# Optimization experiments

Hardware: AMD Instinct MI355X
Metric: run time of the kernel (lower is better)

Reference implementation:

```python
import jax, jax.numpy as jnp
import numpy as np

EPS = 0.1        # entropic regularization
MAX_ITER = 50    # fixed iteration count (torch early-stops on host; we run all iters)
P = 1            # cost exponent
N_POINTS = 4096
D_FEAT = 2


def _cost_matrix(x, y):
    # x: [N, D], y: [M, D] -> C: [N, M], sum_d |x_i - y_j|^p
    return jnp.sum(jnp.abs(x[:, None, :] - y[None, :, :]) ** P, axis=-1)


def setup_inputs() -> dict:
    key = jax.random.key(0)
    k1, k2 = jax.random.split(key)
    x = jax.random.normal(k1, (N_POINTS, D_FEAT), dtype=jnp.float32)
    y = jax.random.normal(k2, (N_POINTS, D_FEAT), dtype=jnp.float32)
    return {"x": x, "y": y}


def reference(x, y):
    n, m = x.shape[0], y.shape[0]
    C = _cost_matrix(x, y)  # [N, M]
    log_mu = jnp.log(jnp.full((n,), 1.0 / n, dtype=x.dtype) + 1e-8)
    log_nu = jnp.log(jnp.full((m,), 1.0 / m, dtype=y.dtype) + 1e-8)

    def M(u, v):
        # modified cost: (-C + u_i + v_j) / eps
        return (-C + u[:, None] + v[None, :]) / EPS

    def step(carry, _):
        u, v = carry
        u = EPS * (log_mu - jax.scipy.special.logsumexp(M(u, v), axis=-1)) + u
        v = EPS * (log_nu - jax.scipy.special.logsumexp(M(u, v), axis=-2)) + v
        return (u, v), None

    u0 = jnp.zeros((n,), dtype=x.dtype)
    v0 = jnp.zeros((m,), dtype=y.dtype)
    (u, v), _ = jax.lax.scan(step, (u0, v0), None, length=MAX_ITER)

    pi = jnp.exp(M(u, v))                 # transport plan [N, M]
    cost = jnp.sum(pi * C)                # scalar (reduction='none', 2D input)
    return cost ** (1.0 / P), pi, C
```

## Files before the change

### kernel.cpp

```cpp
#include <hip/hip_runtime.h>


#define NPTS    4096
#define EPS_F   0.1f
#define S_L2E   14.426950408889634f
#define INV_SL  0.0693147180559945f
#define A_LOGMU (-0.8317725207f)
#define N_ITER  50
#define NBLK    256
#define TPB     1024
#define WPB     (TPB / 64)
#define RPW     2
#define HALFC   2048
#define NJT     (HALFC / 256)
#define NLEAF   16
#define BSTRIDE 64
#define BAR_INTS ((NLEAF + 2) * BSTRIDE)

typedef float f4u __attribute__((ext_vector_type(4), aligned(4)));

__device__ __forceinline__ float fexp2(float x) {
#if __has_builtin(__builtin_amdgcn_exp2f)
  return __builtin_amdgcn_exp2f(x);
#else
  float r;
  asm("v_exp_f32 %0, %1" : "=v"(r) : "v"(x));
  return r;
#endif
}

__device__ __forceinline__ float coh_load(const float* p) {
  return __hip_atomic_load(p, __ATOMIC_RELAXED, __HIP_MEMORY_SCOPE_AGENT);
}
__device__ __forceinline__ void coh_store(float* p, float x) {
  __hip_atomic_store(p, x, __ATOMIC_RELAXED, __HIP_MEMORY_SCOPE_AGENT);
}

__device__ __forceinline__ float wave_sum64(float x) {
#pragma unroll
  for (int off = 32; off > 0; off >>= 1) x += __shfl_xor(x, off, 64);
  return x;
}

__device__ __forceinline__ void grid_barrier(int* bar, int k) {
  __syncthreads();
  if (threadIdx.x == 0) {
    int* leaf = bar + (blockIdx.x & (NLEAF - 1)) * BSTRIDE;
    const int old = __hip_atomic_fetch_add(leaf, 1, __ATOMIC_RELAXED,
                                           __HIP_MEMORY_SCOPE_AGENT);
    if (old == NLEAF * k - 1) {
      int* root = bar + NLEAF * BSTRIDE;
      const int ro = __hip_atomic_fetch_add(root, 1, __ATOMIC_RELAXED,
                                            __HIP_MEMORY_SCOPE_AGENT);
      if (ro == NLEAF * k - 1)
        __hip_atomic_store(bar + (NLEAF + 1) * BSTRIDE, k, __ATOMIC_RELAXED,
                           __HIP_MEMORY_SCOPE_AGENT);
    }
    while (__hip_atomic_load(bar + (NLEAF + 1) * BSTRIDE, __ATOMIC_RELAXED,
                             __HIP_MEMORY_SCOPE_AGENT) < k)
      __builtin_amdgcn_s_sleep(2);
  }
  __syncthreads();
}

__device__ __forceinline__ void stage(const float* __restrict__ win,
                                      const float* __restrict__ colp,
                                      float* __restrict__ sW,
                                      float* __restrict__ sC0,
                                      float* __restrict__ sC1, int tid) {
  const int c = tid * 4;
  const float w0 = coh_load(win + c + 0), w1 = coh_load(win + c + 1);
  const float w2 = coh_load(win + c + 2), w3 = coh_load(win + c + 3);
  const float4 a = ((const float4*)colp)[(c >> 1) + 0];
  const float4 b = ((const float4*)colp)[(c >> 1) + 1];
  float4 W, C0, C1;
  W.x = w0 * S_L2E;  W.y = w1 * S_L2E;  W.z = w2 * S_L2E;  W.w = w3 * S_L2E;
  C0.x = a.x * S_L2E; C0.y = a.z * S_L2E; C0.z = b.x * S_L2E; C0.w = b.z * S_L2E;
  C1.x = a.y * S_L2E; C1.y = a.w * S_L2E; C1.z = b.y * S_L2E; C1.w = b.w * S_L2E;
  *(float4*)(sW + c)  = W;
  *(float4*)(sC0 + c) = C0;
  *(float4*)(sC1 + c) = C1;
  __syncthreads();
}

__device__ __forceinline__ void phase(const float* __restrict__ rx,
                                      const float* __restrict__ ry,
                                      const float* __restrict__ sW,
                                      const float* __restrict__ sC0,
                                      const float* __restrict__ sC1,
                                      float (*sPart)[RPW],
                                      float* __restrict__ wout,
                                      int row0blk, int wv, int lane, int tid) {
  const int base = (wv & 1) * HALFC + lane * 4;
  float acc0 = 0.f, acc1 = 0.f;
#pragma unroll
  for (int jt = 0; jt < NJT; ++jt) {
    const int j = base + jt * 256;
    const float4 W  = *(const float4*)(sW + j);
    const float4 C0 = *(const float4*)(sC0 + j);
    const float4 C1 = *(const float4*)(sC1 + j);
    {
      const float a0 = (W.x - fabsf(rx[0] - C0.x)) - fabsf(ry[0] - C1.x);
      const float a1 = (W.y - fabsf(rx[0] - C0.y)) - fabsf(ry[0] - C1.y);
      const float a2 = (W.z - fabsf(rx[0] - C0.z)) - fabsf(ry[0] - C1.z);
      const float a3 = (W.w - fabsf(rx[0] - C0.w)) - fabsf(ry[0] - C1.w);
      acc0 += (fexp2(a0) + fexp2(a1)) + (fexp2(a2) + fexp2(a3));
    }
    {
      const float a0 = (W.x - fabsf(rx[1] - C0.x)) - fabsf(ry[1] - C1.x);
      const float a1 = (W.y - fabsf(rx[1] - C0.y)) - fabsf(ry[1] - C1.y);
      const float a2 = (W.z - fabsf(rx[1] - C0.z)) - fabsf(ry[1] - C1.z);
      const float a3 = (W.w - fabsf(rx[1] - C0.w)) - fabsf(ry[1] - C1.w);
      acc1 += (fexp2(a0) + fexp2(a1)) + (fexp2(a2) + fexp2(a3));
    }
  }
  const float S0 = wave_sum64(acc0);
  const float S1 = wave_sum64(acc1);
  if (lane == 0) { sPart[wv][0] = S0; sPart[wv][1] = S1; }
  __syncthreads();
  if (tid < 16) {
    const int p = tid >> 1, r = tid & 1;
    const float S = sPart[2 * p][r] + sPart[2 * p + 1][r];
    coh_store(wout + row0blk + p * RPW + r, A_LOGMU - EPS_F * __logf(S));
  }
}

__global__ void __launch_bounds__(TPB, 4)
sinkhorn_main(const float* __restrict__ x, const float* __restrict__ y,
              float* __restrict__ u, float* __restrict__ v,
              float* __restrict__ out, int* __restrict__ bar) {
  __shared__ float sW[NPTS], sC0[NPTS], sC1[NPTS];
  __shared__ float sPart[WPB][RPW];
  __shared__ float sCost[WPB];

  const int tid  = threadIdx.x;
  const int wv   = tid >> 6;
  const int lane = tid & 63;
  const int row0blk = blockIdx.x * (WPB / 2) * RPW;
  const int row0 = row0blk + (wv >> 1) * RPW;

  float rxu[RPW], ryu[RPW], rxv[RPW], ryv[RPW];
#pragma unroll
  for (int r = 0; r < RPW; ++r) {
    const float2 xr = ((const float2*)x)[row0 + r];
    const float2 yr = ((const float2*)y)[row0 + r];
    rxu[r] = xr.x * S_L2E;  ryu[r] = xr.y * S_L2E;
    rxv[r] = yr.x * S_L2E;  ryv[r] = yr.y * S_L2E;
  }

  int k = 0;
  for (int it = 0; it < N_ITER; ++it) {
    stage(v, y, sW, sC0, sC1, tid);
    phase(rxu, ryu, sW, sC0, sC1, sPart, u, row0blk, wv, lane, tid);
    grid_barrier(bar, ++k);
    stage(u, x, sW, sC0, sC1, tid);
    phase(rxv, ryv, sW, sC0, sC1, sPart, v, row0blk, wv, lane, tid);
    grid_barrier(bar, ++k);
  }
  stage(v, y, sW, sC0, sC1, tid);

  float* __restrict__ pi = out + 1;
  float* __restrict__ cm = out + 1 + (size_t)NPTS * NPTS;
  float uu[RPW];
#pragma unroll
  for (int r = 0; r < RPW; ++r) uu[r] = coh_load(u + row0 + r) * S_L2E;

  const int base = (wv & 1) * HALFC + lane * 4;
  float costacc = 0.f;
#pragma unroll 2
  for (int jt = 0; jt < NJT; ++jt) {
    const int j = base + jt * 256;
    const float4 W  = *(const float4*)(sW + j);
    const float4 C0 = *(const float4*)(sC0 + j);
    const float4 C1 = *(const float4*)(sC1 + j);
#pragma unroll
    for (int r = 0; r < RPW; ++r) {
      const float s0 = fabsf(rxu[r] - C0.x) + fabsf(ryu[r] - C1.x);
      const float s1 = fabsf(rxu[r] - C0.y) + fabsf(ryu[r] - C1.y);
      const float s2 = fabsf(rxu[r] - C0.z) + fabsf(ryu[r] - C1.z);
      const float s3 = fabsf(rxu[r] - C0.w) + fabsf(ryu[r] - C1.w);
      const float p0 = fexp2((uu[r] + W.x) - s0);
      const float p1 = fexp2((uu[r] + W.y) - s1);
      const float p2 = fexp2((uu[r] + W.z) - s2);
      const float p3 = fexp2((uu[r] + W.w) - s3);
      costacc = fmaf(p0, s0, costacc);
      costacc = fmaf(p1, s1, costacc);
      costacc = fmaf(p2, s2, costacc);
      costacc = fmaf(p3, s3, costacc);
      const size_t off = (size_t)(row0 + r) * NPTS + j;
      f4u pv; pv.x = p0; pv.y = p1; pv.z = p2; pv.w = p3;
      f4u cv; cv.x = s0 * INV_SL; cv.y = s1 * INV_SL;
      cv.z = s2 * INV_SL; cv.w = s3 * INV_SL;
      *(f4u*)(pi + off) = pv;
      *(f4u*)(cm + off) = cv;
    }
  }
  const float cw = wave_sum64(costacc);
  if (lane == 0) sCost[wv] = cw;
  __syncthreads();
  if (tid == 0) {
    float c = 0.f;
#pragma unroll
    for (int w = 0; w < WPB; ++w) c += sCost[w];
    atomicAdd(out, c * INV_SL);
  }
}

__global__ void sinkhorn_init(float* __restrict__ v, int* __restrict__ bar,
                              float* __restrict__ out) {
  const int i = blockIdx.x * blockDim.x + threadIdx.x;
  if (i < NPTS) coh_store(v + i, 0.f);
  if (i < BAR_INTS)
    __hip_atomic_store(bar + i, 0, __ATOMIC_RELAXED, __HIP_MEMORY_SCOPE_AGENT);
  if (i == 0) out[0] = 0.f;
}

extern "C" void kernel_launch(void* const* d_in, const int* in_sizes, int n_in,
                              void* d_out, int out_size, void* d_ws, size_t ws_size,
                              hipStream_t stream) {
  const float* x = (const float*)d_in[0];
  const float* y = (const float*)d_in[1];
  float* u = (float*)d_ws;
  float* v = u + NPTS;
  int* bar = (int*)(v + NPTS);
  float* out = (float*)d_out;

  sinkhorn_init<<<dim3(16), dim3(256), 0, stream>>>(v, bar, out);

  void* args[6];
  args[0] = (void*)&x;
  args[1] = (void*)&y;
  args[2] = (void*)&u;
  args[3] = (void*)&v;
  args[4] = (void*)&out;
  args[5] = (void*)&bar;
  hipLaunchCooperativeKernel((void*)sinkhorn_main, dim3(NBLK), dim3(TPB),
                             args, 0, stream);
}
```

Measured before the change: 750.8 us.

## Cache row-phase cost tile in registers and stage coordinates once

Each thread computes its cost values for the u-update once and keeps them in 64 registers, so the u-phase no longer recomputes the absolute differences every iteration. The x and y coordinates are staged into separate shared-memory arrays once before the loop, and each iteration stages only the dual vector. The grid barrier now spreads the release flag across per-leaf replicas so waiting blocks poll different addresses, and it sleeps for a shorter interval. The cost is higher register pressure at 1024 threads per block and more shared memory, which could reduce occupancy or cause spills.

After: 700.7 us. -6.7%, faster.

```diff
diff --git a/kernel.cpp b/kernel.cpp
--- a/kernel.cpp
+++ b/kernel.cpp
@@ -15,7 +15,7 @@
 #define NJT     (HALFC / 256)
 #define NLEAF   16
 #define BSTRIDE 64
-#define BAR_INTS ((NLEAF + 2) * BSTRIDE)
+#define BAR_INTS ((NLEAF + 1 + NLEAF) * BSTRIDE)
 
 typedef float f4u __attribute__((ext_vector_type(4), aligned(4)));
 
@@ -52,46 +52,81 @@
       int* root = bar + NLEAF * BSTRIDE;
       const int ro = __hip_atomic_fetch_add(root, 1, __ATOMIC_RELAXED,
                                             __HIP_MEMORY_SCOPE_AGENT);
-      if (ro == NLEAF * k - 1)
-        __hip_atomic_store(bar + (NLEAF + 1) * BSTRIDE, k, __ATOMIC_RELAXED,
-                           __HIP_MEMORY_SCOPE_AGENT);
-    }
-    while (__hip_atomic_load(bar + (NLEAF + 1) * BSTRIDE, __ATOMIC_RELAXED,
+      if (ro == NLEAF * k - 1) {
+#pragma unroll
+        for (int rr = 0; rr < NLEAF; ++rr)
+          __hip_atomic_store(bar + (NLEAF + 1 + rr) * BSTRIDE, k,
+                             __ATOMIC_RELAXED, __HIP_MEMORY_SCOPE_AGENT);
+      }
+    }
+    int* rep = bar + (NLEAF + 1 + (blockIdx.x & (NLEAF - 1))) * BSTRIDE;
+    while (__hip_atomic_load(rep, __ATOMIC_RELAXED,
                              __HIP_MEMORY_SCOPE_AGENT) < k)
-      __builtin_amdgcn_s_sleep(2);
-  }
-  __syncthreads();
-}
-
-__device__ __forceinline__ void stage(const float* __restrict__ win,
-                                      const float* __restrict__ colp,
-                                      float* __restrict__ sW,
-                                      float* __restrict__ sC0,
-                                      float* __restrict__ sC1, int tid) {
+      __builtin_amdgcn_s_sleep(1);
+  }
+  __syncthreads();
+}
+
+__device__ __forceinline__ void stageW(const float* __restrict__ win,
+                                       float* __restrict__ sW, int tid) {
   const int c = tid * 4;
   const float w0 = coh_load(win + c + 0), w1 = coh_load(win + c + 1);
   const float w2 = coh_load(win + c + 2), w3 = coh_load(win + c + 3);
+  float4 W;
+  W.x = w0 * S_L2E;  W.y = w1 * S_L2E;  W.z = w2 * S_L2E;  W.w = w3 * S_L2E;
+  *(float4*)(sW + c) = W;
+  __syncthreads();
+}
+
+__device__ __forceinline__ void stageCoords(const float* __restrict__ colp,
+                                            float* __restrict__ sC0,
+                                            float* __restrict__ sC1, int tid) {
+  const int c = tid * 4;
   const float4 a = ((const float4*)colp)[(c >> 1) + 0];
   const float4 b = ((const float4*)colp)[(c >> 1) + 1];
-  float4 W, C0, C1;
-  W.x = w0 * S_L2E;  W.y = w1 * S_L2E;  W.z = w2 * S_L2E;  W.w = w3 * S_L2E;
+  float4 C0, C1;
   C0.x = a.x * S_L2E; C0.y = a.z * S_L2E; C0.z = b.x * S_L2E; C0.w = b.z * S_L2E;
   C1.x = a.y * S_L2E; C1.y = a.w * S_L2E; C1.z = b.y * S_L2E; C1.w = b.w * S_L2E;
-  *(float4*)(sW + c)  = W;
   *(float4*)(sC0 + c) = C0;
   *(float4*)(sC1 + c) = C1;
-  __syncthreads();
-}
-
-__device__ __forceinline__ void phase(const float* __restrict__ rx,
-                                      const float* __restrict__ ry,
-                                      const float* __restrict__ sW,
-                                      const float* __restrict__ sC0,
-                                      const float* __restrict__ sC1,
-                                      float (*sPart)[RPW],
-                                      float* __restrict__ wout,
-                                      int row0blk, int wv, int lane, int tid) {
-  const int base = (wv & 1) * HALFC + lane * 4;
+}
+
+__device__ __forceinline__ void phaseU(const float* __restrict__ sW,
+                                       const float (&Dreg)[NJT][RPW][4],
+                                       float (*sPart)[RPW],
+                                       float* __restrict__ wout,
+                                       int row0blk, int wv, int lane, int tid,
+                                       int base) {
+  float acc0 = 0.f, acc1 = 0.f;
+#pragma unroll
+  for (int jt = 0; jt < NJT; ++jt) {
+    const int j = base + jt * 256;
+    const float4 W = *(const float4*)(sW + j);
+    acc0 += (fexp2(W.x - Dreg[jt][0][0]) + fexp2(W.y - Dreg[jt][0][1])) +
+            (fexp2(W.z - Dreg[jt][0][2]) + fexp2(W.w - Dreg[jt][0][3]));
+    acc1 += (fexp2(W.x - Dreg[jt][1][0]) + fexp2(W.y - Dreg[jt][1][1])) +
+            (fexp2(W.z - Dreg[jt][1][2]) + fexp2(W.w - Dreg[jt][1][3]));
+  }
+  const float S0 = wave_sum64(acc0);
+  const float S1 = wave_sum64(acc1);
+  if (lane == 0) { sPart[wv][0] = S0; sPart[wv][1] = S1; }
+  __syncthreads();
+  if (tid < 16) {
+    const int p = tid >> 1, r = tid & 1;
+    const float S = sPart[2 * p][r] + sPart[2 * p + 1][r];
+    coh_store(wout + row0blk + p * RPW + r, A_LOGMU - EPS_F * __logf(S));
+  }
+}
+
+__device__ __forceinline__ void phaseV(const float* __restrict__ rx,
+                                       const float* __restrict__ ry,
+                                       const float* __restrict__ sW,
+                                       const float* __restrict__ sC0,
+                                       const float* __restrict__ sC1,
+                                       float (*sPart)[RPW],
+                                       float* __restrict__ wout,
+                                       int row0blk, int wv, int lane, int tid,
+                                       int base) {
   float acc0 = 0.f, acc1 = 0.f;
 #pragma unroll
   for (int jt = 0; jt < NJT; ++jt) {
@@ -129,7 +164,9 @@
 sinkhorn_main(const float* __restrict__ x, const float* __restrict__ y,
               float* __restrict__ u, float* __restrict__ v,
               float* __restrict__ out, int* __restrict__ bar) {
-  __shared__ float sW[NPTS], sC0[NPTS], sC1[NPTS];
+  __shared__ float sW[NPTS];
+  __shared__ float sC0y[NPTS], sC1y[NPTS];
+  __shared__ float sC0x[NPTS], sC1x[NPTS];
   __shared__ float sPart[WPB][RPW];
   __shared__ float sCost[WPB];
 
@@ -138,6 +175,7 @@
   const int lane = tid & 63;
   const int row0blk = blockIdx.x * (WPB / 2) * RPW;
   const int row0 = row0blk + (wv >> 1) * RPW;
+  const int base = (wv & 1) * HALFC + lane * 4;
 
   float rxu[RPW], ryu[RPW], rxv[RPW], ryv[RPW];
 #pragma unroll
@@ -148,16 +186,35 @@
     rxv[r] = yr.x * S_L2E;  ryv[r] = yr.y * S_L2E;
   }
 
+  stageCoords(y, sC0y, sC1y, tid);
+  stageCoords(x, sC0x, sC1x, tid);
+  __syncthreads();
+
+  float Dreg[NJT][RPW][4];
+#pragma unroll
+  for (int jt = 0; jt < NJT; ++jt) {
+    const int j = base + jt * 256;
+    const float4 C0 = *(const float4*)(sC0y + j);
+    const float4 C1 = *(const float4*)(sC1y + j);
+#pragma unroll
+    for (int r = 0; r < RPW; ++r) {
+      Dreg[jt][r][0] = fabsf(rxu[r] - C0.x) + fabsf(ryu[r] - C1.x);
+      Dreg[jt][r][1] = fabsf(rxu[r] - C0.y) + fabsf(ryu[r] - C1.y);
+      Dreg[jt][r][2] = fabsf(rxu[r] - C0.z) + fabsf(ryu[r] - C1.z);
+      Dreg[jt][r][3] = fabsf(rxu[r] - C0.w) + fabsf(ryu[r] - C1.w);
+    }
+  }
+
   int k = 0;
   for (int it = 0; it < N_ITER; ++it) {
-    stage(v, y, sW, sC0, sC1, tid);
-    phase(rxu, ryu, sW, sC0, sC1, sPart, u, row0blk, wv, lane, tid);
+    stageW(v, sW, tid);
+    phaseU(sW, Dreg, sPart, u, row0blk, wv, lane, tid, base);
     grid_barrier(bar, ++k);
-    stage(u, x, sW, sC0, sC1, tid);
-    phase(rxv, ryv, sW, sC0, sC1, sPart, v, row0blk, wv, lane, tid);
+    stageW(u, sW, tid);
+    phaseV(rxv, ryv, sW, sC0x, sC1x, sPart, v, row0blk, wv, lane, tid, base);
     grid_barrier(bar, ++k);
   }
-  stage(v, y, sW, sC0, sC1, tid);
+  stageW(v, sW, tid);
 
   float* __restrict__ pi = out + 1;
   float* __restrict__ cm = out + 1 + (size_t)NPTS * NPTS;
@@ -165,20 +222,17 @@
 #pragma unroll
   for (int r = 0; r < RPW; ++r) uu[r] = coh_load(u + row0 + r) * S_L2E;
 
-  const int base = (wv & 1) * HALFC + lane * 4;
   float costacc = 0.f;
-#pragma unroll 2
-  for (int jt = 0; jt < NJT; ++jt) {
-    const int j = base + jt * 256;
-    const float4 W  = *(const float4*)(sW + j);
-    const float4 C0 = *(const float4*)(sC0 + j);
-    const float4 C1 = *(const float4*)(sC1 + j);
+#pragma unroll
+  for (int jt = 0; jt < NJT; ++jt) {
+    const int j = base + jt * 256;
+    const float4 W = *(const float4*)(sW + j);
 #pragma unroll
     for (int r = 0; r < RPW; ++r) {
-      const float s0 = fabsf(rxu[r] - C0.x) + fabsf(ryu[r] - C1.x);
-      const float s1 = fabsf(rxu[r] - C0.y) + fabsf(ryu[r] - C1.y);
-      const float s2 = fabsf(rxu[r] - C0.z) + fabsf(ryu[r] - C1.z);
-      const float s3 = fabsf(rxu[r] - C0.w) + fabsf(ryu[r] - C1.w);
+      const float s0 = Dreg[jt][r][0];
+      const float s1 = Dreg[jt][r][1];
+      const float s2 = Dreg[jt][r][2];
+      const float s3 = Dreg[jt][r][3];
       const float p0 = fexp2((uu[r] + W.x) - s0);
       const float p1 = fexp2((uu[r] + W.y) - s1);
       const float p2 = fexp2((uu[r] + W.z) - s2);
```
